# Kernel optimization log

Measured on AMD Instinct MI355X. Metric: run time of the kernel, lower is better.

Reference implementation:

```python
import jax, jax.numpy as jnp
import numpy as np

EMB_DIM = 400
NUM_ENT = 100000
NUM_REL = 200
OUT_CH = 6
STRIDE = 2
MAX_ARITY = 3
ARITY = 3
BATCH = 8192
W_OUT = (EMB_DIM - 1) // STRIDE + 1          # conv output width (filt_w=1, stride=2)
FC_LEN = OUT_CH * W_OUT                      # 1200


def setup_inputs() -> dict:
    key = jax.random.key(0)
    ks = jax.random.split(key, 10)
    r_idx = jax.random.randint(ks[0], (BATCH,), 0, NUM_REL)
    E_mat = jax.random.randint(ks[1], (BATCH, ARITY), 0, NUM_ENT)
    ms = jax.random.normal(ks[2], (BATCH, ARITY), dtype=jnp.float32)
    bs = jax.random.normal(ks[3], (BATCH, ARITY), dtype=jnp.float32)
    E_emb = jax.random.normal(ks[4], (NUM_ENT, EMB_DIM), dtype=jnp.float32) * 0.05
    R_emb = jax.random.normal(ks[5], (NUM_REL, EMB_DIM), dtype=jnp.float32) * 0.05
    fc2_W = jax.random.normal(ks[6], (OUT_CH, MAX_ARITY + 1), dtype=jnp.float32) * 0.1
    fc2_b = jax.random.normal(ks[7], (OUT_CH,), dtype=jnp.float32) * 0.1
    fc_W = jax.random.normal(ks[8], (EMB_DIM, FC_LEN), dtype=jnp.float32) * 0.02
    fc_b = jax.random.normal(ks[9], (EMB_DIM,), dtype=jnp.float32) * 0.02
    return {"r_idx": r_idx, "E_mat": E_mat, "ms": ms, "bs": bs,
            "E_emb": E_emb, "R_emb": R_emb,
            "fc2_W": fc2_W, "fc2_b": fc2_b, "fc_W": fc_W, "fc_b": fc_b}


def _convolve(E_emb, fc2_W, fc2_b, fc_W, fc_b, e_idx, pos):
    # Embedding gather: (B, D)
    e = E_emb[e_idx]
    # 1x1 grouped conv with stride=2 == strided slice of the embedding: (B, W_OUT)
    e_s = e[:, ::STRIDE]
    # Hypernetwork filter from fc2(one_hot(pos)) -- identical across batch: (OUT_CH,)
    k = fc2_W[:, pos] + fc2_b
    # Per-sample outer product, flattened oc-major (matches torch view order): (B, FC_LEN)
    feat = (k[None, :, None] * e_s[:, None, :]).reshape(e.shape[0], FC_LEN)
    # fc: Linear(FC_LEN, EMB_DIM)
    return jnp.einsum('bf,df->bd', feat, fc_W) + fc_b


def reference(r_idx, E_mat, ms, bs, E_emb, R_emb, fc2_W, fc2_b, fc_W, fc_b):
    r = R_emb[r_idx]                                        # (B, D)
    x = None
    for i in range(E_mat.shape[1]):                         # small fixed arity loop
        e = _convolve(E_emb, fc2_W, fc2_b, fc_W, fc_b, E_mat[:, i], i)
        e = e * ms[:, i][:, None] + bs[:, i][:, None]
        x = e if x is None else x * e
    x = x * r
    return jnp.sum(x, axis=1)                               # (B,)
```

## Files before the change

### kernel.cpp

```cpp
#include <hip/hip_runtime.h>

typedef __attribute__((ext_vector_type(8))) short bf16x8;
typedef __attribute__((ext_vector_type(4))) float f32x4;

#define EMB_DIM 400
#define OUT_CH  6
#define ARITY   3
#define BATCH   8192
#define W_OUT   200
#define FC_LEN  1200
#define NT      25
#define NKS     7
#define BM      32
#define NTASK   (ARITY * BM * 100)
#define NLD     19

static __device__ __forceinline__ ushort f2bf(float f) {
    union { float f; uint u; } v; v.f = f;
    uint u = v.u;
    return (ushort)((u + 0x7FFF + ((u >> 16) & 1)) >> 16);
}

__global__ __launch_bounds__(256)
void pack_M(const float* __restrict__ fc2_W, const float* __restrict__ fc2_b,
            const float* __restrict__ fc_W, ushort* __restrict__ Mb) {
    __shared__ float Bt[32][16];
    const int bid = blockIdx.x;
    const int kk  = blockIdx.y;
    const int i = bid / NT, t = bid % NT;
    float kc[OUT_CH];
#pragma unroll
    for (int c = 0; c < OUT_CH; ++c) kc[c] = fc2_W[c * 4 + i] + fc2_b[c];
    const int tid = threadIdx.x;
    const int dd = tid >> 4, wl = tid & 15;
    const int d = t * 16 + dd;
#pragma unroll
    for (int s = 0; s < 2; ++s) {
        int w = kk * 32 + wl + 16 * s;
        float v = 0.f;
        if (w < W_OUT) {
#pragma unroll
            for (int c = 0; c < OUT_CH; ++c)
                v = fmaf(kc[c], fc_W[d * FC_LEN + c * W_OUT + w], v);
        }
        Bt[wl + 16 * s][dd] = v;
    }
    __syncthreads();
    if (tid < 64) {
        const int l = tid;
        ushort vals[8];
#pragma unroll
        for (int j = 0; j < 8; ++j)
            vals[j] = f2bf(Bt[(l >> 4) * 8 + j][l & 15]);
        *reinterpret_cast<uint4*>(Mb + ((size_t)(bid * NKS + kk) * 64 + l) * 8) =
            *reinterpret_cast<const uint4*>(vals);
    }
}

__global__ __launch_bounds__(512)
void hype_mfma(const int* __restrict__ r_idx, const int* __restrict__ E_mat,
               const float* __restrict__ ms, const float* __restrict__ bs,
               const float* __restrict__ E_emb, const float* __restrict__ R_emb,
               const float* __restrict__ fc_b, const ushort* __restrict__ Mb,
               float* __restrict__ out) {
    __shared__ ushort es[ARITY * 2 * NKS * 64 * 8];
    __shared__ float sm_ms[BM * 3], sm_bs[BM * 3], sm_fcb[EMB_DIM];
    __shared__ int   sm_rb[BM], sm_ent[BM * 3];
    __shared__ float osum[4][BM];

    const int tid = threadIdx.x;
    const int b0 = blockIdx.x * BM;

    if (tid < BM * 3) {
        sm_ms[tid]  = ms[b0 * 3 + tid];
        sm_bs[tid]  = bs[b0 * 3 + tid];
        sm_ent[tid] = E_mat[b0 * 3 + tid];
    }
    if (tid >= 96 && tid < 96 + BM) sm_rb[tid - 96] = r_idx[b0 + tid - 96] * EMB_DIM;
    for (int z = tid; z < EMB_DIM; z += 512) sm_fcb[z] = fc_b[z];

    uint* esu = reinterpret_cast<uint*>(es);
    for (int z = tid; z < ARITY * 2 * 192; z += 512) {
        int pair = z / 192, off = z % 192;
        esu[(pair * NKS + 6) * 256 + 64 + off] = 0;
    }
    __syncthreads();

    float4 vreg[NLD];
#pragma unroll
    for (int k = 0; k < NLD; ++k) {
        int tq = tid + k * 512;
        if (tq < NTASK) {
            int q = tq % 100;
            int p = tq / 100;
            int i = p / BM, r = p % BM;
            int ent = sm_ent[r * 3 + i];
            vreg[k] = *reinterpret_cast<const float4*>(
                E_emb + (size_t)ent * EMB_DIM + 4 * q);
        }
    }
#pragma unroll
    for (int k = 0; k < NLD; ++k) {
        int tq = tid + k * 512;
        if (tq < NTASK) {
            int q = tq % 100;
            int p = tq / 100;
            int i = p / BM, r = p % BM;
            int w = 2 * q;
            int kk = w >> 5;
            int lsub = (w >> 3) & 3;
            int j = w & 7;
            int rg = r >> 4, rl = r & 15;
            int l = lsub * 16 + rl;
            uint pk = (uint)f2bf(vreg[k].x) | ((uint)f2bf(vreg[k].z) << 16);
            esu[(((i * 2 + rg) * NKS + kk) * 64 + l) * 4 + (j >> 1)] = pk;
        }
    }
    __syncthreads();

    const int wid = tid >> 6;
    const int lane = tid & 63;
    const int rg = wid & 1, cg = wid >> 1;
    const int cl = lane & 15;
    const int rql = lane >> 4;

    bf16x8 afrag[ARITY][NKS];
#pragma unroll
    for (int i = 0; i < ARITY; ++i)
#pragma unroll
        for (int kk = 0; kk < NKS; ++kk)
            afrag[i][kk] = *reinterpret_cast<const bf16x8*>(
                es + (((i * 2 + rg) * NKS + kk) * 64 + lane) * 8);

    float msv[ARITY][4], bsv[ARITY][4];
    int rbv[4];
#pragma unroll
    for (int r_ = 0; r_ < 4; ++r_) {
        int row = rg * 16 + rql * 4 + r_;
#pragma unroll
        for (int i = 0; i < ARITY; ++i) {
            msv[i][r_] = sm_ms[row * 3 + i];
            bsv[i][r_] = sm_bs[row * 3 + i];
        }
        rbv[r_] = sm_rb[row];
    }

    float rowsum[4] = {0.f, 0.f, 0.f, 0.f};
    for (int t = cg; t < NT; t += 4) {
        f32x4 acc[ARITY];
#pragma unroll
        for (int i = 0; i < ARITY; ++i) {
            f32x4 a = {0.f, 0.f, 0.f, 0.f};
            const ushort* bp = Mb + ((size_t)(i * NT + t) * NKS * 64 + lane) * 8;
#pragma unroll
            for (int kk = 0; kk < NKS; ++kk) {
                bf16x8 bfr = *reinterpret_cast<const bf16x8*>(bp + kk * 512);
                a = __builtin_amdgcn_mfma_f32_16x16x32_bf16(afrag[i][kk], bfr, a, 0, 0, 0);
            }
            acc[i] = a;
        }
        const int d = t * 16 + cl;
        const float fcb = sm_fcb[d];
#pragma unroll
        for (int r_ = 0; r_ < 4; ++r_) {
            float Rr = R_emb[rbv[r_] + d];
            float e0 = fmaf(acc[0][r_] + fcb, msv[0][r_], bsv[0][r_]);
            float e1 = fmaf(acc[1][r_] + fcb, msv[1][r_], bsv[1][r_]);
            float e2 = fmaf(acc[2][r_] + fcb, msv[2][r_], bsv[2][r_]);
            rowsum[r_] = fmaf(e0 * e1 * e2, Rr, rowsum[r_]);
        }
    }

#pragma unroll
    for (int m = 1; m < 16; m <<= 1)
#pragma unroll
        for (int r_ = 0; r_ < 4; ++r_)
            rowsum[r_] += __shfl_xor(rowsum[r_], m, 64);
    if (cl == 0) {
#pragma unroll
        for (int r_ = 0; r_ < 4; ++r_)
            osum[cg][rg * 16 + rql * 4 + r_] = rowsum[r_];
    }
    __syncthreads();
    if (tid < BM)
        out[b0 + tid] = osum[0][tid] + osum[1][tid] + osum[2][tid] + osum[3][tid];
}

extern "C" void kernel_launch(void* const* d_in, const int* in_sizes, int n_in,
                              void* d_out, int out_size, void* d_ws, size_t ws_size,
                              hipStream_t stream) {
    const int*   r_idx = (const int*)d_in[0];
    const int*   E_mat = (const int*)d_in[1];
    const float* ms    = (const float*)d_in[2];
    const float* bs    = (const float*)d_in[3];
    const float* E_emb = (const float*)d_in[4];
    const float* R_emb = (const float*)d_in[5];
    const float* fc2_W = (const float*)d_in[6];
    const float* fc2_b = (const float*)d_in[7];
    const float* fc_W  = (const float*)d_in[8];
    const float* fc_b  = (const float*)d_in[9];
    float*  out = (float*)d_out;
    ushort* Mb  = (ushort*)d_ws;

    pack_M<<<dim3(ARITY * NT, NKS), 256, 0, stream>>>(fc2_W, fc2_b, fc_W, Mb);
    hype_mfma<<<BATCH / BM, 512, 0, stream>>>(r_idx, E_mat, ms, bs, E_emb, R_emb,
                                              fc_b, Mb, out);
}
```

Measured before the change: 34.08 us.

## Split K across wave pairs so each B fragment feeds both row groups

Waves are now paired by K-half instead of by row group. Each wave loads only half of the B (Mb) K-slices and multiplies them against both 16-row A groups, which halves global B traffic per wave. Partial sums for the other row group are exchanged through double-buffered shared memory with a block-wide barrier every step. In exchange the kernel adds per-iteration __syncthreads, LDS traffic, and uneven K work, since one half has 4 slices and the other has 3.

```diff
diff --git a/kernel.cpp b/kernel.cpp
--- a/kernel.cpp
+++ b/kernel.cpp
@@ -64,6 +64,7 @@
                const float* __restrict__ fc_b, const ushort* __restrict__ Mb,
                float* __restrict__ out) {
     __shared__ ushort es[ARITY * 2 * NKS * 64 * 8];
+    __shared__ f32x4  exch[2][4][2][ARITY][64];
     __shared__ float sm_ms[BM * 3], sm_bs[BM * 3], sm_fcb[EMB_DIM];
     __shared__ int   sm_rb[BM], sm_ent[BM * 3];
     __shared__ float osum[4][BM];
@@ -118,25 +119,31 @@
     }
     __syncthreads();
 
-    const int wid = tid >> 6;
+    const int wid  = tid >> 6;
     const int lane = tid & 63;
-    const int rg = wid & 1, cg = wid >> 1;
-    const int cl = lane & 15;
-    const int rql = lane >> 4;
-
-    bf16x8 afrag[ARITY][NKS];
+    const int kg   = wid & 1;
+    const int cg   = wid >> 1;
+    const int cl   = lane & 15;
+    const int rql  = lane >> 4;
+    const int kb   = kg * 4;
+
+    bf16x8 aOwn[ARITY][4] = {}, aOth[ARITY][4] = {};
 #pragma unroll
     for (int i = 0; i < ARITY; ++i)
 #pragma unroll
-        for (int kk = 0; kk < NKS; ++kk)
-            afrag[i][kk] = *reinterpret_cast<const bf16x8*>(
-                es + (((i * 2 + rg) * NKS + kk) * 64 + lane) * 8);
+        for (int kkh = 0; kkh < 4; ++kkh)
+            if (kkh < 3 || kg == 0) {
+                aOwn[i][kkh] = *reinterpret_cast<const bf16x8*>(
+                    es + (((i * 2 + kg) * NKS + kb + kkh) * 64 + lane) * 8);
+                aOth[i][kkh] = *reinterpret_cast<const bf16x8*>(
+                    es + (((i * 2 + (1 - kg)) * NKS + kb + kkh) * 64 + lane) * 8);
+            }
 
     float msv[ARITY][4], bsv[ARITY][4];
     int rbv[4];
 #pragma unroll
     for (int r_ = 0; r_ < 4; ++r_) {
-        int row = rg * 16 + rql * 4 + r_;
+        int row = kg * 16 + rql * 4 + r_;
 #pragma unroll
         for (int i = 0; i < ARITY; ++i) {
             msv[i][r_] = sm_ms[row * 3 + i];
@@ -146,28 +153,49 @@
     }
 
     float rowsum[4] = {0.f, 0.f, 0.f, 0.f};
-    for (int t = cg; t < NT; t += 4) {
-        f32x4 acc[ARITY];
+#pragma unroll 1
+    for (int step = 0; step < 7; ++step) {
+        const int t = cg + 4 * step;
+        f32x4 own[ARITY], oth[ARITY];
 #pragma unroll
         for (int i = 0; i < ARITY; ++i) {
-            f32x4 a = {0.f, 0.f, 0.f, 0.f};
-            const ushort* bp = Mb + ((size_t)(i * NT + t) * NKS * 64 + lane) * 8;
-#pragma unroll
-            for (int kk = 0; kk < NKS; ++kk) {
-                bf16x8 bfr = *reinterpret_cast<const bf16x8*>(bp + kk * 512);
-                a = __builtin_amdgcn_mfma_f32_16x16x32_bf16(afrag[i][kk], bfr, a, 0, 0, 0);
+            own[i] = (f32x4){0.f, 0.f, 0.f, 0.f};
+            oth[i] = (f32x4){0.f, 0.f, 0.f, 0.f};
+        }
+        if (t < NT) {
+#pragma unroll
+            for (int i = 0; i < ARITY; ++i) {
+                const ushort* bp = Mb + (size_t)(i * NT + t) * NKS * 512
+                                      + kb * 512 + lane * 8;
+#pragma unroll
+                for (int kkh = 0; kkh < 4; ++kkh)
+                    if (kkh < 3 || kg == 0) {
+                        bf16x8 bfr = *reinterpret_cast<const bf16x8*>(bp + kkh * 512);
+                        own[i] = __builtin_amdgcn_mfma_f32_16x16x32_bf16(
+                            aOwn[i][kkh], bfr, own[i], 0, 0, 0);
+                        oth[i] = __builtin_amdgcn_mfma_f32_16x16x32_bf16(
+                            aOth[i][kkh], bfr, oth[i], 0, 0, 0);
+                    }
             }
-            acc[i] = a;
-        }
-        const int d = t * 16 + cl;
-        const float fcb = sm_fcb[d];
-#pragma unroll
-        for (int r_ = 0; r_ < 4; ++r_) {
-            float Rr = R_emb[rbv[r_] + d];
-            float e0 = fmaf(acc[0][r_] + fcb, msv[0][r_], bsv[0][r_]);
-            float e1 = fmaf(acc[1][r_] + fcb, msv[1][r_], bsv[1][r_]);
-            float e2 = fmaf(acc[2][r_] + fcb, msv[2][r_], bsv[2][r_]);
-            rowsum[r_] = fmaf(e0 * e1 * e2, Rr, rowsum[r_]);
+#pragma unroll
+            for (int i = 0; i < ARITY; ++i)
+                exch[step & 1][cg][kg][i][lane] = oth[i];
+        }
+        __syncthreads();
+        if (t < NT) {
+            f32x4 a0 = own[0] + exch[step & 1][cg][1 - kg][0][lane];
+            f32x4 a1 = own[1] + exch[step & 1][cg][1 - kg][1][lane];
+            f32x4 a2 = own[2] + exch[step & 1][cg][1 - kg][2][lane];
+            const int d = t * 16 + cl;
+            const float fcb = sm_fcb[d];
+#pragma unroll
+            for (int r_ = 0; r_ < 4; ++r_) {
+                float Rr = R_emb[rbv[r_] + d];
+                float e0 = fmaf(a0[r_] + fcb, msv[0][r_], bsv[0][r_]);
+                float e1 = fmaf(a1[r_] + fcb, msv[1][r_], bsv[1][r_]);
+                float e2 = fmaf(a2[r_] + fcb, msv[2][r_], bsv[2][r_]);
+                rowsum[r_] = fmaf(e0 * e1 * e2, Rr, rowsum[r_]);
+            }
         }
     }
 
@@ -179,7 +207,7 @@
     if (cl == 0) {
 #pragma unroll
         for (int r_ = 0; r_ < 4; ++r_)
-            osum[cg][rg * 16 + rql * 4 + r_] = rowsum[r_];
+            osum[cg][kg * 16 + rql * 4 + r_] = rowsum[r_];
     }
     __syncthreads();
     if (tid < BM)
```

New measurement: 38.91 us. 1.14x slower.
